# Performance work log

Hardware: AMD Instinct MI355X
Metric: run time of the kernel (lower is better)

Reference implementation:

```python
import jax, jax.numpy as jnp
import numpy as np

PAD_INDEX = 0
SMOOTHING = 0.1


def setup_inputs() -> dict:
    key = jax.random.key(0)
    k1, k2 = jax.random.split(key)
    B, T, V = 4, 1024, 32000
    # log-probabilities over the vocab (KLDivLoss expects log-space inputs)
    log_probs = jax.nn.log_softmax(jax.random.normal(k1, (B, T, V), dtype=jnp.float32), axis=-1)
    trg = jax.random.randint(k2, (B, T), 0, V)
    return {"log_probs": log_probs, "trg": trg}


def reference(log_probs, trg):
    # Fused label-smoothed KL divergence (sum reduction), mathematically identical to
    # building the smoothed distribution q and computing sum(q * (log q - log_probs)):
    #   q[t]       = 1 - smoothing                      (target column)
    #   q[pad]     = 0                                  (pad column)
    #   q[other]   = smoothing / (V - 2)
    #   rows where target == pad contribute 0.
    V = log_probs.shape[-1]
    lp = log_probs.reshape(-1, V)          # [N, V]
    t = trg.reshape(-1)                    # [N]

    conf = 1.0 - SMOOTHING                 # mass on the true token
    sm = SMOOTHING / (V - 2)               # mass on every other non-pad token
    log_conf = float(np.log(conf))
    log_sm = float(np.log(sm))

    lp_t = jnp.take_along_axis(lp, t[:, None], axis=1)[:, 0]   # [N] log p(target)
    lp_pad = lp[:, PAD_INDEX]                                   # [N] log p(pad)
    lp_sum = jnp.sum(lp, axis=-1)                               # [N] sum_v log p(v)

    # per-row KL: conf*(log conf - lp_t) + sm * sum_{v != t, v != pad} (log sm - lp_v)
    row = (conf * (log_conf - lp_t)
           + sm * (V - 2) * log_sm
           - sm * (lp_sum - lp_t - lp_pad))

    mask = (t != PAD_INDEX).astype(lp.dtype)
    return jnp.sum(row * mask)
```

## Files before the change

### kernel.cpp

```cpp
#include <hip/hip_runtime.h>
#include <math.h>


#define SMOOTHING 0.1

__global__ __launch_bounds__(256) void xent_row_kernel(
    const float* __restrict__ lp, const int* __restrict__ trg,
    float* __restrict__ row_out, int V) {
  const int row = blockIdx.x;
  const float* rp = lp + (size_t)row * (size_t)V;
  const int tid = threadIdx.x;

  float s = 0.0f;
  const int nvec = V >> 2;
  const float4* rp4 = reinterpret_cast<const float4*>(rp);
  for (int i = tid; i < nvec; i += 256) {
    float4 v = rp4[i];
    s += (v.x + v.y) + (v.z + v.w);
  }
  for (int i = (nvec << 2) + tid; i < V; i += 256) s += rp[i];

  #pragma unroll
  for (int off = 32; off > 0; off >>= 1) s += __shfl_down(s, off, 64);

  __shared__ float wsum[4];
  const int lane = tid & 63;
  const int wave = tid >> 6;
  if (lane == 0) wsum[wave] = s;
  __syncthreads();

  if (tid == 0) {
    float lp_sum = wsum[0] + wsum[1] + wsum[2] + wsum[3];
    const int t = trg[row];
    const float lp_t = rp[t];
    const float lp_pad = rp[0];

    const double conf = 1.0 - SMOOTHING;
    const double sm = SMOOTHING / (double)(V - 2);
    const double log_conf = log(conf);
    const double log_sm = log(sm);

    double rv = conf * (log_conf - (double)lp_t)
              + sm * (double)(V - 2) * log_sm
              - sm * ((double)lp_sum - (double)lp_t - (double)lp_pad);
    row_out[row] = (t != 0) ? (float)rv : 0.0f;
  }
}

__global__ __launch_bounds__(256) void xent_final_sum(
    const float* __restrict__ rows, float* __restrict__ out, int n) {
  const int tid = threadIdx.x;
  float s = 0.0f;
  for (int i = tid; i < n; i += 256) s += rows[i];

  #pragma unroll
  for (int off = 32; off > 0; off >>= 1) s += __shfl_down(s, off, 64);

  __shared__ float wsum[4];
  const int lane = tid & 63;
  const int wave = tid >> 6;
  if (lane == 0) wsum[wave] = s;
  __syncthreads();

  if (tid == 0) out[0] = wsum[0] + wsum[1] + wsum[2] + wsum[3];
}

extern "C" void kernel_launch(void* const* d_in, const int* in_sizes, int n_in,
                              void* d_out, int out_size, void* d_ws, size_t ws_size,
                              hipStream_t stream) {
  const float* lp = (const float*)d_in[0];
  const int* trg = (const int*)d_in[1];
  float* out = (float*)d_out;

  const int rows = in_sizes[1];
  const int V = in_sizes[0] / rows;

  float* row_out = (float*)d_ws;

  xent_row_kernel<<<rows, 256, 0, stream>>>(lp, trg, row_out, V);
  xent_final_sum<<<1, 256, 0, stream>>>(row_out, out, rows);
}
```

Baseline: 98.79 us.

## Fuse final reduction via last-block atomic counter and unroll nontemporal row loads

Merges the row kernel and the single-block final sum into one kernel: each block publishes its row value, bumps a global counter, and the last block to finish sums all row values. The row loop is unrolled four ways with independent accumulators and nontemporal vector loads to keep more memory requests in flight. A hipMemsetAsync clears the counter each call, so one kernel launch is traded for a memset, and the last block adds a serial tail.

```diff
diff --git a/kernel.cpp b/kernel.cpp
--- a/kernel.cpp
+++ b/kernel.cpp
@@ -4,26 +4,42 @@
 
 #define SMOOTHING 0.1
 
-__global__ __launch_bounds__(256) void xent_row_kernel(
+typedef float f32x4 __attribute__((ext_vector_type(4)));
+
+__global__ __launch_bounds__(256) void xent_fused_kernel(
     const float* __restrict__ lp, const int* __restrict__ trg,
-    float* __restrict__ row_out, int V) {
+    float* __restrict__ row_out, unsigned int* __restrict__ counter,
+    float* __restrict__ out, int V, int rows) {
   const int row = blockIdx.x;
   const float* rp = lp + (size_t)row * (size_t)V;
   const int tid = threadIdx.x;
 
-  float s = 0.0f;
   const int nvec = V >> 2;
-  const float4* rp4 = reinterpret_cast<const float4*>(rp);
-  for (int i = tid; i < nvec; i += 256) {
-    float4 v = rp4[i];
-    s += (v.x + v.y) + (v.z + v.w);
+  const f32x4* rp4 = reinterpret_cast<const f32x4*>(rp);
+  float s0 = 0.0f, s1 = 0.0f, s2 = 0.0f, s3 = 0.0f;
+  int i = tid;
+  for (; i + 768 < nvec; i += 1024) {
+    f32x4 a = __builtin_nontemporal_load(&rp4[i]);
+    f32x4 b = __builtin_nontemporal_load(&rp4[i + 256]);
+    f32x4 c = __builtin_nontemporal_load(&rp4[i + 512]);
+    f32x4 d = __builtin_nontemporal_load(&rp4[i + 768]);
+    s0 += (a.x + a.y) + (a.z + a.w);
+    s1 += (b.x + b.y) + (b.z + b.w);
+    s2 += (c.x + c.y) + (c.z + c.w);
+    s3 += (d.x + d.y) + (d.z + d.w);
   }
-  for (int i = (nvec << 2) + tid; i < V; i += 256) s += rp[i];
+  for (; i < nvec; i += 256) {
+    f32x4 v = __builtin_nontemporal_load(&rp4[i]);
+    s0 += (v.x + v.y) + (v.z + v.w);
+  }
+  for (int j = (nvec << 2) + tid; j < V; j += 256) s0 += rp[j];
+  float s = (s0 + s1) + (s2 + s3);
 
   #pragma unroll
   for (int off = 32; off > 0; off >>= 1) s += __shfl_down(s, off, 64);
 
   __shared__ float wsum[4];
+  __shared__ bool amLast;
   const int lane = tid & 63;
   const int wave = tid >> 6;
   if (lane == 0) wsum[wave] = s;
@@ -43,26 +59,30 @@
     double rv = conf * (log_conf - (double)lp_t)
               + sm * (double)(V - 2) * log_sm
               - sm * ((double)lp_sum - (double)lp_t - (double)lp_pad);
-    row_out[row] = (t != 0) ? (float)rv : 0.0f;
+    float rvf = (t != 0) ? (float)rv : 0.0f;
+
+    __hip_atomic_store(&row_out[row], rvf, __ATOMIC_RELAXED,
+                       __HIP_MEMORY_SCOPE_AGENT);
+    __threadfence();
+    unsigned prev = atomicAdd(counter, 1u);
+    amLast = (prev == (unsigned)(rows - 1));
   }
-}
-
-__global__ __launch_bounds__(256) void xent_final_sum(
-    const float* __restrict__ rows, float* __restrict__ out, int n) {
-  const int tid = threadIdx.x;
-  float s = 0.0f;
-  for (int i = tid; i < n; i += 256) s += rows[i];
-
-  #pragma unroll
-  for (int off = 32; off > 0; off >>= 1) s += __shfl_down(s, off, 64);
-
-  __shared__ float wsum[4];
-  const int lane = tid & 63;
-  const int wave = tid >> 6;
-  if (lane == 0) wsum[wave] = s;
   __syncthreads();
 
-  if (tid == 0) out[0] = wsum[0] + wsum[1] + wsum[2] + wsum[3];
+  if (amLast) {
+    __threadfence();
+    float t = 0.0f;
+    for (int j = tid; j < rows; j += 256) {
+      t += __hip_atomic_load(&row_out[j], __ATOMIC_RELAXED,
+                             __HIP_MEMORY_SCOPE_AGENT);
+    }
+    #pragma unroll
+    for (int off = 32; off > 0; off >>= 1) t += __shfl_down(t, off, 64);
+    __shared__ float fsum[4];
+    if (lane == 0) fsum[wave] = t;
+    __syncthreads();
+    if (tid == 0) out[0] = fsum[0] + fsum[1] + fsum[2] + fsum[3];
+  }
 }
 
 extern "C" void kernel_launch(void* const* d_in, const int* in_sizes, int n_in,
@@ -76,7 +96,10 @@
   const int V = in_sizes[0] / rows;
 
   float* row_out = (float*)d_ws;
+  unsigned int* counter =
+      (unsigned int*)((char*)d_ws + (((size_t)rows * 4 + 255) & ~(size_t)255));
 
-  xent_row_kernel<<<rows, 256, 0, stream>>>(lp, trg, row_out, V);
-  xent_final_sum<<<1, 256, 0, stream>>>(row_out, out, rows);
+  (void)hipMemsetAsync(counter, 0, sizeof(unsigned int), stream);
+  xent_fused_kernel<<<rows, 256, 0, stream>>>(lp, trg, row_out, counter, out,
+                                              V, rows);
 }
```

Result: slower. 288.4 us (+191.9%).
